# Performance work log

Measured on AMD Instinct MI355X. Metric: run time of the kernel, lower is better.

## Reference

```python
import jax, jax.numpy as jnp
import numpy as np

IMG = 416                      # image_shape
DIST = 1075.0                  # isocenter_distance
N_ANG = 320                    # 360 / rotation_resolution(=1.125 deg)
N_DET = IMG                    # detector bins
N_SAMP = IMG                   # integration samples per ray
SCALE = 512.0 / 416.0 * 0.03   # self.scale


def _ray_coords():
    """Pixel-space sample coordinates for every (angle, detector, sample).
    Returns cols, rows of shape [N_ANG, N_DET, N_SAMP] and the step length dt."""
    thetas = (jnp.arange(N_ANG, dtype=jnp.float32) * np.float32(2.0 * np.pi / N_ANG))
    half_diag = (IMG / 2.0) * np.sqrt(2.0)
    gamma_max = np.float32(np.arcsin(half_diag / DIST))  # half fan angle covering image
    gammas = jnp.linspace(-gamma_max, gamma_max, N_DET, dtype=jnp.float32)
    ray_len = np.float32(IMG * np.sqrt(2.0))             # chord length through image
    ts = jnp.linspace(np.float32(DIST - ray_len / 2.0),
                      np.float32(DIST + ray_len / 2.0), N_SAMP, dtype=jnp.float32)
    dt = float(ray_len / (N_SAMP - 1))

    th = thetas[:, None, None]        # [A,1,1]
    gm = gammas[None, :, None]        # [1,D,1]
    t = ts[None, None, :]             # [1,1,S]
    # source position on circle of radius DIST, ray direction toward detector
    sx = np.float32(DIST) * jnp.cos(th)
    sy = np.float32(DIST) * jnp.sin(th)
    x = sx - t * jnp.cos(th + gm)     # [A,D,S] world coords (isocenter at origin)
    y = sy - t * jnp.sin(th + gm)
    ctr = np.float32((IMG - 1) / 2.0)
    return x + ctr, y + ctr, dt       # pixel (col, row) coordinates


def _bilinear(img, cols, rows):
    """Zero-padded bilinear sampling of img[H,W] at float (row,col) coords."""
    c0 = jnp.floor(cols)
    r0 = jnp.floor(rows)
    wc = cols - c0
    wr = rows - r0
    c0i = c0.astype(jnp.int32)
    r0i = r0.astype(jnp.int32)

    def g(ri, ci):
        inb = (ri >= 0) & (ri < IMG) & (ci >= 0) & (ci < IMG)
        v = img[jnp.clip(ri, 0, IMG - 1), jnp.clip(ci, 0, IMG - 1)]
        return jnp.where(inb, v, jnp.float32(0.0))

    return (g(r0i, c0i) * (1 - wr) * (1 - wc)
            + g(r0i, c0i + 1) * (1 - wr) * wc
            + g(r0i + 1, c0i) * wr * (1 - wc)
            + g(r0i + 1, c0i + 1) * wr * wc)


def fan_beam_fp(vol):
    """vol: [B,H,W] -> sinogram [B, N_ANG, N_DET] via ray integration."""
    cols, rows, dt = _ray_coords()
    proj_one = lambda img: _bilinear(img, cols, rows).sum(axis=-1) * jnp.float32(dt)
    return jax.vmap(proj_one)(vol)


def setup_inputs() -> dict:
    key = jax.random.key(0)
    k1, k2 = jax.random.split(key)
    inp = jax.random.normal(k1, (1, 1, IMG, IMG), dtype=jnp.float32)
    tgt = jax.random.normal(k2, (1, 1, IMG, IMG), dtype=jnp.float32)
    return {"input": inp, "target": tgt}


def reference(input, target):
    input_proj = fan_beam_fp(input[:, 0])   # squeeze(1)
    target_proj = fan_beam_fp(target[:, 0])
    return jnp.mean((input_proj - target_proj) ** 2) * jnp.float32(SCALE)
```

## Files before the change

kernel.cpp:

```cpp
#include <hip/hip_runtime.h>
#include <math.h>

#define IMG 416
#define N_ANG 320
#define N_DET 416
#define N_SAMP 416

#define GSTRIDE 464
#define GROWS   432
#define GBYTES  ((size_t)GROWS * GSTRIDE)
#define GWORDS  (GROWS * GSTRIDE / 4)

#define SPLANE  (N_ANG * N_DET)
#define SBYTES  ((size_t)4 * SPLANE * sizeof(float))
#define WSNEED  (GBYTES + SBYTES)

#define LSTRIDE_W 59
#define LROWS     229
#define LWORDS    (LROWS * LSTRIDE_W)

typedef float vfloat2 __attribute__((ext_vector_type(2)));

__global__ __launch_bounds__(256) void pack_kernel(const float* __restrict__ a,
                                                   const float* __restrict__ b,
                                                   unsigned int* __restrict__ G,
                                                   float* __restrict__ out) {
    int i = blockIdx.x * 256 + threadIdx.x;
    if (i == 0) out[0] = 0.0f;
    if (i >= GWORDS) return;
    int pr = i / (GSTRIDE / 4);
    int wc = i - pr * (GSTRIDE / 4);
    int r  = pr - 8;
    int c0 = wc * 4 - 8;
    float v[4];
    #pragma unroll
    for (int j = 0; j < 4; ++j) {
        int c = c0 + j;
        float val = 0.0f;
        if ((unsigned)r < (unsigned)IMG && (unsigned)c < (unsigned)IMG) {
            int idx = r * IMG + c;
            val = a[idx] - b[idx];
        }
        v[j] = val;
    }
    unsigned int u = __builtin_amdgcn_cvt_pk_fp8_f32(v[0], v[1], 0u, false);
    u = __builtin_amdgcn_cvt_pk_fp8_f32(v[2], v[3], u, true);
    G[i] = u;
}

__global__ void zero_out_kernel(float* __restrict__ out) {
    if (threadIdx.x == 0) out[0] = 0.0f;
}

__global__ __launch_bounds__(448) void proj_lds(const unsigned int* __restrict__ G,
                                                float* __restrict__ S,
                                                float theta_step, float gmax,
                                                float gstep, float t0,
                                                float dtstep) {
    __shared__ unsigned int Lw[LWORDS];

    const int blk = blockIdx.x;
    const int a  = blk >> 2;
    const int q  = blk & 3;
    const int qi = q >> 1, qj = q & 1;
    const int r0 = qi ? 222 : -2;
    const int c0 = qj ? 220 : -4;
    const int nrows = (qi ? 197 : 227) + 2;

    {
        const int gbase = ((r0 + 8) * GSTRIDE + (c0 + 8)) >> 2;
        const int total = nrows * LSTRIDE_W;
        for (int i = threadIdx.x; i < total; i += 448) {
            int rr = i / LSTRIDE_W;
            int cc = i - rr * LSTRIDE_W;
            Lw[rr * LSTRIDE_W + cc] = G[gbase + rr * 116 + cc];
        }
    }
    __syncthreads();

    const int d = threadIdx.x;
    if (d < N_DET) {
        const float theta = (float)a * theta_step;
        const float gamma = fmaf((float)d, gstep, -gmax);
        float s1, c1, s2, c2;
        sincosf(theta, &s1, &c1);
        sincosf(theta + gamma, &s2, &c2);
        const float sx = fmaf(1075.0f, c1, 207.5f);
        const float sy = fmaf(1075.0f, s1, 207.5f);

        const float C0 = fmaf(-t0, c2, sx), dc = dtstep * c2;
        const float R0 = fmaf(-t0, s2, sy), dr = dtstep * s2;

        const float cl = qj ? 224.0f : -1.0f, ch = qj ? 416.0f : 224.0f;
        const float rl = qi ? 224.0f : -1.0f, rh = qi ? 416.0f : 224.0f;

        int klo = 0, khi = N_SAMP - 1;
        auto clip1 = [&](float X0, float dX, float lo, float hi) {
            if (fabsf(dX) < 1e-8f) {
                if (!(X0 >= lo && X0 < hi)) { klo = 1; khi = 0; }
            } else {
                const float inv = 1.0f / dX;
                float x1 = (X0 - hi) * inv;
                float x2 = (X0 - lo) * inv;
                x1 = fminf(fmaxf(x1, -1e6f), 1e6f);
                x2 = fminf(fmaxf(x2, -1e6f), 1e6f);
                int lo_k, hi_k;
                if (dX > 0.0f) { lo_k = (int)floorf(x1) + 1; hi_k = (int)floorf(x2); }
                else           { lo_k = (int)ceilf(x2);      hi_k = (int)ceilf(x1) - 1; }
                klo = max(klo, lo_k);
                khi = min(khi, hi_k);
            }
        };
        clip1(C0, dc, cl, ch);
        clip1(R0, dr, rl, rh);

        float acc = 0.0f;
        if (klo <= khi) {
            float colR = fmaf(-(float)klo, dc, C0) - (float)c0;
            float rowR = fmaf(-(float)klo, dr, R0) - (float)r0;
            #pragma unroll 4
            for (int k = klo; k <= khi; ++k) {
                const int ci = (int)colR;
                const int ri = (int)rowR;
                const float wc = colR - (float)ci;
                const float wr = rowR - (float)ri;
                const int widx = ri * LSTRIDE_W + (ci >> 2);
                const unsigned int d00 = Lw[widx];
                const unsigned int d10 = Lw[widx + LSTRIDE_W];
                const unsigned int d01 = Lw[widx + 1];
                const unsigned int d11 = Lw[widx + LSTRIDE_W + 1];
                const int sh8 = (ci & 3) << 3;
                const unsigned int r0w =
                    (unsigned int)(((((unsigned long long)d01) << 32) | d00) >> sh8);
                const unsigned int r1w =
                    (unsigned int)(((((unsigned long long)d11) << 32) | d10) >> sh8);
                const vfloat2 t2 = __builtin_amdgcn_cvt_pk_f32_fp8(r0w, false);
                const vfloat2 b2 = __builtin_amdgcn_cvt_pk_f32_fp8(r1w, false);
                const float top = fmaf(wc, t2[1] - t2[0], t2[0]);
                const float bot = fmaf(wc, b2[1] - b2[0], b2[0]);
                acc = fmaf(wr, bot - top, acc + top);
                colR -= dc;
                rowR -= dr;
            }
        }
        S[q * SPLANE + a * N_DET + d] = acc;
    }
}

__global__ __launch_bounds__(256) void reduce_kernel(const float* __restrict__ S,
                                                     float* __restrict__ out,
                                                     float coef) {
    const int i = blockIdx.x * 256 + threadIdx.x;
    float v = 0.0f;
    if (i < SPLANE)
        v = (S[i] + S[SPLANE + i]) + (S[2 * SPLANE + i] + S[3 * SPLANE + i]);
    float sq = v * v;
    #pragma unroll
    for (int m = 32; m > 0; m >>= 1) sq += __shfl_down(sq, m, 64);
    __shared__ float w[4];
    const int lane = threadIdx.x & 63;
    if (lane == 0) w[threadIdx.x >> 6] = sq;
    __syncthreads();
    if (threadIdx.x == 0)
        atomicAdd(out, (w[0] + w[1] + w[2] + w[3]) * coef);
}

__global__ __launch_bounds__(256) void proj_fused(const float* __restrict__ imgA,
                                                  const float* __restrict__ imgB,
                                                  float* __restrict__ out,
                                                  float theta_step, float gmax,
                                                  float gstep, float t0,
                                                  float dtstep, float coef) {
    const int idx = blockIdx.x * 256 + threadIdx.x;
    const int a  = idx / N_DET;
    const int dd = idx - a * N_DET;
    const float theta = (float)a * theta_step;
    const float gamma = fmaf((float)dd, gstep, -gmax);
    float s1, c1, s2, c2;
    sincosf(theta, &s1, &c1);
    sincosf(theta + gamma, &s2, &c2);
    const float sx = 1075.0f * c1 + 207.5f;
    const float sy = 1075.0f * s1 + 207.5f;
    float acc = 0.0f;
    #pragma unroll 4
    for (int s = 0; s < N_SAMP; ++s) {
        const float t   = fmaf((float)s, dtstep, t0);
        const float col = fmaf(-t, c2, sx);
        const float row = fmaf(-t, s2, sy);
        const float c0 = floorf(col);
        const float r0 = floorf(row);
        const float wc = col - c0;
        const float wr = row - r0;
        const int ci = (int)c0;
        const int ri = (int)r0;
        auto Gv = [&](int r, int c) -> float {
            if ((unsigned)r < (unsigned)IMG && (unsigned)c < (unsigned)IMG)
                return imgA[r * IMG + c] - imgB[r * IMG + c];
            return 0.0f;
        };
        const float v00 = Gv(ri, ci);
        const float v01 = Gv(ri, ci + 1);
        const float v10 = Gv(ri + 1, ci);
        const float v11 = Gv(ri + 1, ci + 1);
        const float top = fmaf(wc, v01 - v00, v00);
        const float bot = fmaf(wc, v11 - v10, v10);
        acc += fmaf(wr, bot - top, top);
    }
    float sq = acc * acc;
    #pragma unroll
    for (int o = 32; o > 0; o >>= 1) sq += __shfl_down(sq, o, 64);
    __shared__ float wsum[4];
    const int lane = threadIdx.x & 63;
    if (lane == 0) wsum[threadIdx.x >> 6] = sq;
    __syncthreads();
    if (threadIdx.x == 0)
        atomicAdd(out, (wsum[0] + wsum[1] + wsum[2] + wsum[3]) * coef);
}

extern "C" void kernel_launch(void* const* d_in, const int* in_sizes, int n_in,
                              void* d_out, int out_size, void* d_ws, size_t ws_size,
                              hipStream_t stream) {
    const float* in = (const float*)d_in[0];
    const float* tg = (const float*)d_in[1];
    float* out = (float*)d_out;

    const double half_diag = (IMG / 2.0) * sqrt(2.0);
    const double ray_len   = IMG * sqrt(2.0);
    const float  gmax      = (float)asin(half_diag / 1075.0);
    const float  gstep     = (float)(2.0 * (double)gmax / (N_DET - 1));
    const float  t0        = (float)(1075.0 - ray_len / 2.0);
    const float  dtstep    = (float)(ray_len / (N_SAMP - 1));
    const float  theta_step = (float)(2.0 * M_PI / N_ANG);
    const double dt        = ray_len / (N_SAMP - 1);
    const double SCALE     = 512.0 / 416.0 * 0.03;
    const float  coef      = (float)(dt * dt * SCALE / ((double)N_ANG * N_DET));

    if (ws_size >= WSNEED) {
        unsigned int* G = (unsigned int*)d_ws;
        float* S = (float*)((char*)d_ws + GBYTES);
        pack_kernel<<<(GWORDS + 255) / 256, 256, 0, stream>>>(in, tg, G, out);
        proj_lds<<<N_ANG * 4, 448, 0, stream>>>(G, S, theta_step, gmax, gstep,
                                                t0, dtstep);
        reduce_kernel<<<(SPLANE + 255) / 256, 256, 0, stream>>>(S, out, coef);
    } else {
        zero_out_kernel<<<1, 64, 0, stream>>>(out);
        proj_fused<<<(N_ANG * N_DET) / 256, 256, 0, stream>>>(
            in, tg, out, theta_step, gmax, gstep, t0, dtstep, coef);
    }
}
```

Measured before the change: 110.5 us.

## Fuse reduction into projection kernel via atomics and last-block finalize

```diff
diff --git a/kernel.cpp b/kernel.cpp
--- a/kernel.cpp
+++ b/kernel.cpp
@@ -12,21 +12,27 @@
 #define GWORDS  (GROWS * GSTRIDE / 4)
 
 #define SPLANE  (N_ANG * N_DET)
-#define SBYTES  ((size_t)4 * SPLANE * sizeof(float))
-#define WSNEED  (GBYTES + SBYTES)
+#define S1BYTES ((size_t)SPLANE * 4)
+#define WSNEED  (GBYTES + S1BYTES + 64)
 
 #define LSTRIDE_W 59
+#define LSTRIDE_B (LSTRIDE_W * 4)
 #define LROWS     229
 #define LWORDS    (LROWS * LSTRIDE_W)
+
+#define NBLK (N_ANG * 4)
 
 typedef float vfloat2 __attribute__((ext_vector_type(2)));
 
 __global__ __launch_bounds__(256) void pack_kernel(const float* __restrict__ a,
                                                    const float* __restrict__ b,
                                                    unsigned int* __restrict__ G,
+                                                   float* __restrict__ S,
+                                                   unsigned int* __restrict__ cnt,
                                                    float* __restrict__ out) {
     int i = blockIdx.x * 256 + threadIdx.x;
-    if (i == 0) out[0] = 0.0f;
+    if (i == 0) { out[0] = 0.0f; *cnt = 0u; }
+    if (i < SPLANE) S[i] = 0.0f;
     if (i >= GWORDS) return;
     int pr = i / (GSTRIDE / 4);
     int wc = i - pr * (GSTRIDE / 4);
@@ -54,10 +60,14 @@
 
 __global__ __launch_bounds__(448) void proj_lds(const unsigned int* __restrict__ G,
                                                 float* __restrict__ S,
+                                                unsigned int* __restrict__ cnt,
+                                                float* __restrict__ out,
                                                 float theta_step, float gmax,
                                                 float gstep, float t0,
-                                                float dtstep) {
+                                                float dtstep, float coef) {
     __shared__ unsigned int Lw[LWORDS];
+    __shared__ float wsum[7];
+    __shared__ int lastFlag;
 
     const int blk = blockIdx.x;
     const int a  = blk >> 2;
@@ -114,55 +124,61 @@
         clip1(C0, dc, cl, ch);
         clip1(R0, dr, rl, rh);
 
-        float acc = 0.0f;
         if (klo <= khi) {
             float colR = fmaf(-(float)klo, dc, C0) - (float)c0;
             float rowR = fmaf(-(float)klo, dr, R0) - (float)r0;
+            const unsigned char* __restrict__ Lb = (const unsigned char*)Lw;
+            float acc = 0.0f;
             #pragma unroll 4
             for (int k = klo; k <= khi; ++k) {
                 const int ci = (int)colR;
                 const int ri = (int)rowR;
                 const float wc = colR - (float)ci;
                 const float wr = rowR - (float)ri;
-                const int widx = ri * LSTRIDE_W + (ci >> 2);
-                const unsigned int d00 = Lw[widx];
-                const unsigned int d10 = Lw[widx + LSTRIDE_W];
-                const unsigned int d01 = Lw[widx + 1];
-                const unsigned int d11 = Lw[widx + LSTRIDE_W + 1];
-                const int sh8 = (ci & 3) << 3;
-                const unsigned int r0w =
-                    (unsigned int)(((((unsigned long long)d01) << 32) | d00) >> sh8);
-                const unsigned int r1w =
-                    (unsigned int)(((((unsigned long long)d11) << 32) | d10) >> sh8);
-                const vfloat2 t2 = __builtin_amdgcn_cvt_pk_f32_fp8(r0w, false);
-                const vfloat2 b2 = __builtin_amdgcn_cvt_pk_f32_fp8(r1w, false);
+                const int base = ri * LSTRIDE_B + ci;
+                const unsigned int b00 = Lb[base];
+                const unsigned int b01 = Lb[base + 1];
+                const unsigned int b10 = Lb[base + LSTRIDE_B];
+                const unsigned int b11 = Lb[base + LSTRIDE_B + 1];
+                const vfloat2 t2 = __builtin_amdgcn_cvt_pk_f32_fp8(b00 | (b01 << 8), false);
+                const vfloat2 b2 = __builtin_amdgcn_cvt_pk_f32_fp8(b10 | (b11 << 8), false);
                 const float top = fmaf(wc, t2[1] - t2[0], t2[0]);
                 const float bot = fmaf(wc, b2[1] - b2[0], b2[0]);
                 acc = fmaf(wr, bot - top, acc + top);
                 colR -= dc;
                 rowR -= dr;
             }
-        }
-        S[q * SPLANE + a * N_DET + d] = acc;
-    }
-}
-
-__global__ __launch_bounds__(256) void reduce_kernel(const float* __restrict__ S,
-                                                     float* __restrict__ out,
-                                                     float coef) {
-    const int i = blockIdx.x * 256 + threadIdx.x;
-    float v = 0.0f;
-    if (i < SPLANE)
-        v = (S[i] + S[SPLANE + i]) + (S[2 * SPLANE + i] + S[3 * SPLANE + i]);
-    float sq = v * v;
-    #pragma unroll
-    for (int m = 32; m > 0; m >>= 1) sq += __shfl_down(sq, m, 64);
-    __shared__ float w[4];
-    const int lane = threadIdx.x & 63;
-    if (lane == 0) w[threadIdx.x >> 6] = sq;
-    __syncthreads();
-    if (threadIdx.x == 0)
-        atomicAdd(out, (w[0] + w[1] + w[2] + w[3]) * coef);
+            atomicAdd(&S[a * N_DET + d], acc);
+        }
+    }
+
+    __threadfence();
+    __syncthreads();
+    if (threadIdx.x == 0) {
+        unsigned int old = __hip_atomic_fetch_add(cnt, 1u, __ATOMIC_ACQ_REL,
+                                                  __HIP_MEMORY_SCOPE_AGENT);
+        lastFlag = (old == (unsigned)(NBLK - 1));
+    }
+    __syncthreads();
+    if (lastFlag) {
+        __threadfence();
+        float sq = 0.0f;
+        for (int i = threadIdx.x; i < SPLANE; i += 448) {
+            const float v = __hip_atomic_load(&S[i], __ATOMIC_RELAXED,
+                                              __HIP_MEMORY_SCOPE_AGENT);
+            sq = fmaf(v, v, sq);
+        }
+        #pragma unroll
+        for (int m = 32; m > 0; m >>= 1) sq += __shfl_down(sq, m, 64);
+        if ((threadIdx.x & 63) == 0) wsum[threadIdx.x >> 6] = sq;
+        __syncthreads();
+        if (threadIdx.x == 0) {
+            float t = 0.0f;
+            #pragma unroll
+            for (int w = 0; w < 7; ++w) t += wsum[w];
+            out[0] = t * coef;
+        }
+    }
 }
 
 __global__ __launch_bounds__(256) void proj_fused(const float* __restrict__ imgA,
@@ -238,10 +254,10 @@
     if (ws_size >= WSNEED) {
         unsigned int* G = (unsigned int*)d_ws;
         float* S = (float*)((char*)d_ws + GBYTES);
-        pack_kernel<<<(GWORDS + 255) / 256, 256, 0, stream>>>(in, tg, G, out);
-        proj_lds<<<N_ANG * 4, 448, 0, stream>>>(G, S, theta_step, gmax, gstep,
-                                                t0, dtstep);
-        reduce_kernel<<<(SPLANE + 255) / 256, 256, 0, stream>>>(S, out, coef);
+        unsigned int* cnt = (unsigned int*)((char*)d_ws + GBYTES + S1BYTES);
+        pack_kernel<<<(SPLANE + 255) / 256, 256, 0, stream>>>(in, tg, G, S, cnt, out);
+        proj_lds<<<NBLK, 448, 0, stream>>>(G, S, cnt, out, theta_step, gmax,
+                                           gstep, t0, dtstep, coef);
     } else {
         zero_out_kernel<<<1, 64, 0, stream>>>(out);
         proj_fused<<<(N_ANG * N_DET) / 256, 256, 0, stream>>>(
```

Measured after the change: 280.1 us. +153.4%, slower.
